# Optimization experiments

Measured on AMD Instinct MI355X. Metric: run time of the kernel, lower is better.

The kernel has to match this reference:

```python
import jax, jax.numpy as jnp
import numpy as np

N = 100000       # num nodes
E = 1000000      # num edges
D_IN = 128       # input feature dim
D_H = 64         # hidden = output dim
EPS = 1e-5       # GraphNorm eps
SLOPE = 0.2      # LeakyReLU negative slope


def _glorot(key, shape):
    lim = float(np.sqrt(6.0 / (shape[0] + shape[1])))
    return jax.random.uniform(key, shape, jnp.float32, -lim, lim)


def setup_inputs() -> dict:
    key = jax.random.key(0)
    ks = jax.random.split(key, 6)
    return {
        "x": jax.random.normal(ks[0], (N, D_IN), jnp.float32),
        "edge_index": jax.random.randint(ks[1], (2, E), 0, N),
        "W_in": _glorot(ks[2], (D_IN, D_H)),
        "b_in": jnp.zeros((D_H,), jnp.float32),
        "W1": _glorot(ks[3], (D_H, D_H)),
        "b1": jnp.zeros((D_H,), jnp.float32),
        "gn1_alpha": jnp.ones((D_H,), jnp.float32),
        "gn1_gamma": jnp.ones((D_H,), jnp.float32),
        "gn1_beta": jnp.zeros((D_H,), jnp.float32),
        "W2": _glorot(ks[4], (D_H, D_H)),
        "b2": jnp.zeros((D_H,), jnp.float32),
        "gn2_alpha": jnp.ones((D_H,), jnp.float32),
        "gn2_gamma": jnp.ones((D_H,), jnp.float32),
        "gn2_beta": jnp.zeros((D_H,), jnp.float32),
    }


def gcn_conv(x, W, b, src, dst):
    # GCNConv with added self-loops and symmetric normalization:
    # out = D^{-1/2} (A + I) D^{-1/2} (x W) + b
    xw = x @ W                                                 # [N, D]
    ones = jnp.ones((src.shape[0],), x.dtype)
    deg = jax.ops.segment_sum(ones, dst, num_segments=x.shape[0]) + 1.0  # +1 self-loop
    dinv = jax.lax.rsqrt(deg)                                  # [N]
    coef = dinv[src] * dinv[dst]                               # [E]
    agg = jax.ops.segment_sum(xw[src] * coef[:, None], dst, num_segments=x.shape[0])
    return agg + xw * (dinv * dinv)[:, None] + b


def graph_norm(x, alpha, gamma, beta):
    # PyG GraphNorm over a single graph: per-feature mean/var over all nodes
    mean = jnp.mean(x, axis=0)
    c = x - alpha * mean
    var = jnp.mean(c * c, axis=0)
    return gamma * c * jax.lax.rsqrt(var + EPS) + beta


def reference(x, edge_index, W_in, b_in, W1, b1, gn1_alpha, gn1_gamma, gn1_beta,
              W2, b2, gn2_alpha, gn2_gamma, gn2_beta):
    src, dst = edge_index[0], edge_index[1]
    h = x @ W_in + b_in                                        # input projection
    h = graph_norm(gcn_conv(h, W1, b1, src, dst), gn1_alpha, gn1_gamma, gn1_beta)
    h = jnp.where(h > 0, h, SLOPE * h)                         # LeakyReLU(0.2); dropout=eval (identity)
    h = graph_norm(gcn_conv(h, W2, b2, src, dst), gn2_alpha, gn2_gamma, gn2_beta)
    return h                                                    # [N, D_H]
```

## Files before the change

kernel.cpp:

```cpp
#include <hip/hip_runtime.h>
#include <stdint.h>
#include <string.h>

#define N_NODES 100000
#define N_EDGES 1000000
#define D_IN 128
#define D_H 64
#define EPS 1e-5f
#define SLOPE 0.2f

typedef unsigned short u16;
typedef unsigned int u32;
typedef __attribute__((ext_vector_type(8))) short bf16x8;
typedef __attribute__((ext_vector_type(4))) float f32x4;

__device__ __forceinline__ float bf2f(u16 u) {
    union { u32 i; float f; } v; v.i = ((u32)u) << 16; return v.f;
}
__device__ __forceinline__ u16 f2bf(float f) {
    union { float f; u32 i; } v; v.f = f;
    u32 r = (v.i + 0x7fffu + ((v.i >> 16) & 1u)) >> 16;
    return (u16)r;
}
__device__ __forceinline__ bool is_f32(const void* flagp) {
    return *(const u32*)flagp == 0x3F800000u;
}
__device__ __forceinline__ float loadf(const void* p, size_t i, bool m) {
    return m ? ((const float*)p)[i] : bf2f(((const u16*)p)[i]);
}

__global__ void kprep(const void* __restrict__ W_in, const void* __restrict__ b_in,
                      const void* __restrict__ W1, const void* __restrict__ W2,
                      const void* __restrict__ flagp,
                      u16* __restrict__ WcT, u16* __restrict__ W2T,
                      float* __restrict__ bc)
{
    bool m = is_f32(flagp);
    int t = threadIdx.x;
    if (blockIdx.x < 64) {
        int c = blockIdx.x;
        __shared__ float w1c[D_H];
        if (t < D_H) w1c[t] = loadf(W1, t * D_H + c, m);
        __syncthreads();
        float acc = 0.f;
        #pragma unroll 8
        for (int j = 0; j < D_H; j++) acc += loadf(W_in, t * D_H + j, m) * w1c[j];
        WcT[c * D_IN + t] = f2bf(acc);
        if (t == 0) {
            float b = 0.f;
            for (int j = 0; j < D_H; j++) b += loadf(b_in, j, m) * w1c[j];
            bc[c] = b;
        }
    } else {
        int idx = (blockIdx.x - 64) * 128 + t;
        int n = idx >> 6, k = idx & 63;
        W2T[n * D_H + k] = f2bf(loadf(W2, k * D_H + n, m));
    }
}

__global__ void kfill(const int* __restrict__ ei, int* __restrict__ cnt,
                      int* __restrict__ bucket)
{
    int e = blockIdx.x * blockDim.x + threadIdx.x;
    if (e >= N_EDGES) return;
    int s = ei[e];
    int d = ei[N_EDGES + e];
    int slot = atomicAdd(&cnt[d], 1);
    if (slot < 64) bucket[(size_t)d * 64 + slot] = s;
}

__global__ void kdinv(const int* __restrict__ cnt, float* __restrict__ dinv,
                      u16* __restrict__ xwb_pad)
{
    int i = blockIdx.x * blockDim.x + threadIdx.x;
    if (i < D_H) xwb_pad[(size_t)N_NODES * D_H + i] = 0;
    if (i >= N_NODES) return;
    dinv[i] = rsqrtf((float)cnt[i] + 1.0f);
}

__global__ __launch_bounds__(256) void kgemm1(const void* __restrict__ x,
        const u16* __restrict__ WcT, const float* __restrict__ bc,
        const float* __restrict__ dinv, const void* __restrict__ flagp,
        u16* __restrict__ xwb)
{
    bool m = is_f32(flagp);
    __shared__ __align__(16) u16 xs[64 * 136];
    __shared__ __align__(16) u16 WT[64 * 136];
    int tid = threadIdx.x;
    int row0 = blockIdx.x * 64;
    for (int i = tid; i < 64 * 32; i += 256) {
        int r = i >> 5, kq = (i & 31) * 4;
        *(ushort4*)(WT + r * 136 + kq) = *(const ushort4*)(WcT + r * D_IN + kq);
    }
    for (int i = tid; i < 64 * 32; i += 256) {
        int r = i >> 5, kq = (i & 31) * 4;
        int gr = row0 + r;
        ushort4 u = make_ushort4(0, 0, 0, 0);
        if (gr < N_NODES) {
            if (m) {
                float4 v = *(const float4*)((const float*)x + (size_t)gr * D_IN + kq);
                u = make_ushort4(f2bf(v.x), f2bf(v.y), f2bf(v.z), f2bf(v.w));
            } else {
                u = *(const ushort4*)((const u16*)x + (size_t)gr * D_IN + kq);
            }
        }
        *(ushort4*)(xs + r * 136 + kq) = u;
    }
    __syncthreads();
    int w = tid >> 6, L = tid & 63;
    int q = L >> 4, c = L & 15;
    f32x4 acc[4];
    #pragma unroll
    for (int ct = 0; ct < 4; ct++) {
        float b = bc[ct * 16 + c];
        acc[ct] = (f32x4){b, b, b, b};
    }
    const u16* ap = xs + (w * 16 + c) * 136 + q * 8;
    #pragma unroll
    for (int kk = 0; kk < 4; kk++) {
        bf16x8 af = *(const bf16x8*)(ap + kk * 32);
        #pragma unroll
        for (int ct = 0; ct < 4; ct++) {
            bf16x8 bfr = *(const bf16x8*)(WT + (ct * 16 + c) * 136 + kk * 32 + q * 8);
            acc[ct] = __builtin_amdgcn_mfma_f32_16x16x32_bf16(af, bfr, acc[ct], 0, 0, 0);
        }
    }
    #pragma unroll
    for (int r = 0; r < 4; r++) {
        int gr = row0 + w * 16 + q * 4 + r;
        if (gr < N_NODES) {
            float ds = dinv[gr];
            #pragma unroll
            for (int ct = 0; ct < 4; ct++)
                xwb[(size_t)gr * D_H + ct * 16 + c] = f2bf(acc[ct][r] * ds);
        }
    }
}

__global__ __launch_bounds__(256) void kagg(const u16* __restrict__ xwb,
        const float* __restrict__ dinv, const int* __restrict__ cnt,
        const int* __restrict__ bucket, const void* __restrict__ bvec,
        const void* __restrict__ flagp, u16* __restrict__ ybuf,
        float* __restrict__ accum)
{
    bool m = is_f32(flagp);
    __shared__ __align__(16) char smem[4][8192];
    __shared__ float red_s[4][64], red_q[4][64];
    int tid = threadIdx.x;
    int wv = tid >> 6, L = tid & 63;
    int half = L >> 5, mm = L & 31;
    int node0 = blockIdx.x * 32 + wv * 8;

    int cnt8 = cnt[node0 + (L & 7)];
    float di8 = dinv[node0 + (L & 7)];
    int deg[8]; float dd[8];
    #pragma unroll
    for (int t = 0; t < 8; t++) {
        deg[t] = min(__builtin_amdgcn_readlane(cnt8, t), 64);
        dd[t] = __uint_as_float(__builtin_amdgcn_readlane(__float_as_uint(di8), t));
    }
    float b0 = loadf(bvec, 2 * mm, m), b1 = loadf(bvec, 2 * mm + 1, m);

    float ls0 = 0, ls1 = 0, lq0 = 0, lq1 = 0;
    char* base = &smem[wv][0];

    #pragma unroll
    for (int b = 0; b < 2; b++) {
        int nb = node0 + b * 4;
        int tl = L >> 4, sl = L & 15;
        int i_l = nb + tl;
        int raw = bucket[(size_t)i_l * 64 + sl];
        int degL = min(__shfl(cnt8, b * 4 + tl), 64);
        int src = (sl < degL) ? raw : ((sl == degL) ? i_l : N_NODES);

        #pragma unroll
        for (int k = 0; k < 8; k++) {
            int srcK = __shfl(src, k * 8 + (L >> 3));
            const u16* gp = xwb + (size_t)srcK * D_H + (L & 7) * 8;
            __builtin_amdgcn_global_load_lds(gp, base + k * 1024, 16, 0, 0);
        }
        __builtin_amdgcn_s_waitcnt(0);
        __builtin_amdgcn_sched_barrier(0);
        asm volatile("" ::: "memory");

        float A0 = 0, A1 = 0, C0 = 0, C1 = 0;
        #pragma unroll
        for (int p = 0; p < 2; p++) {
            int np = p * 2 + half;
            const u32* rp = (const u32*)(base + np * 2048);
            float a0 = 0, a1 = 0;
            #pragma unroll
            for (int s = 0; s < 16; s++) {
                u32 v = rp[s * 32 + mm];
                a0 += __uint_as_float(v << 16);
                a1 += __uint_as_float(v & 0xffff0000u);
            }
            if (p == 0) { A0 = a0; A1 = a1; } else { C0 = a0; C1 = a1; }
        }
        #pragma unroll
        for (int t = 0; t < 4; t++) {
            int degt = deg[b * 4 + t];
            if (degt >= 16) {
                int i = nb + t;
                float r0 = 0, r1 = 0;
                for (int s = 16 + half; s <= degt; s += 2) {
                    int sv = (s < degt) ? bucket[(size_t)i * 64 + s] : i;
                    u32 v = *((const u32*)(xwb + (size_t)sv * D_H) + mm);
                    r0 += __uint_as_float(v << 16);
                    r1 += __uint_as_float(v & 0xffff0000u);
                }
                r0 += __shfl_xor(r0, 32);
                r1 += __shfl_xor(r1, 32);
                bool mine = (half == (t & 1));
                if (t < 2) { A0 += mine ? r0 : 0.f; A1 += mine ? r1 : 0.f; }
                else       { C0 += mine ? r0 : 0.f; C1 += mine ? r1 : 0.f; }
            }
        }
        #pragma unroll
        for (int p = 0; p < 2; p++) {
            float a0 = p ? C0 : A0, a1 = p ? C1 : A1;
            float ddv = half ? dd[b * 4 + p * 2 + 1] : dd[b * 4 + p * 2];
            float y0 = ddv * a0 + b0;
            float y1 = ddv * a1 + b1;
            int node = nb + p * 2 + half;
            ((u32*)(ybuf + (size_t)node * D_H))[mm] =
                (u32)f2bf(y0) | ((u32)f2bf(y1) << 16);
            ls0 += y0; ls1 += y1; lq0 += y0 * y0; lq1 += y1 * y1;
        }
        asm volatile("" ::: "memory");
    }

    ls0 += __shfl_xor(ls0, 32); ls1 += __shfl_xor(ls1, 32);
    lq0 += __shfl_xor(lq0, 32); lq1 += __shfl_xor(lq1, 32);
    if (half == 0) {
        *(float2*)&red_s[wv][2 * mm] = make_float2(ls0, ls1);
        *(float2*)&red_q[wv][2 * mm] = make_float2(lq0, lq1);
    }
    __syncthreads();
    if (tid < 64) {
        atomicAdd(&accum[tid],      red_s[0][tid] + red_s[1][tid] + red_s[2][tid] + red_s[3][tid]);
        atomicAdd(&accum[64 + tid], red_q[0][tid] + red_q[1][tid] + red_q[2][tid] + red_q[3][tid]);
    }
}

__global__ void kparams(const float* __restrict__ accum, const void* __restrict__ alpha,
        const void* __restrict__ gamma, const void* __restrict__ beta,
        const void* __restrict__ flagp, float* __restrict__ params)
{
    bool m = is_f32(flagp);
    int f = threadIdx.x;
    float mean = accum[f] * (1.0f / N_NODES);
    float al = loadf(alpha, f, m);
    float var = accum[64 + f] * (1.0f / N_NODES) - mean * mean * al * (2.0f - al);
    var = fmaxf(var, 0.f);
    float a = loadf(gamma, f, m) * rsqrtf(var + EPS);
    params[f] = a;
    params[64 + f] = loadf(beta, f, m) - a * al * mean;
}

__global__ __launch_bounds__(256) void kgemm2(const u16* __restrict__ y1b,
        const u16* __restrict__ W2T, const float* __restrict__ params,
        const float* __restrict__ dinv, u16* __restrict__ xwb)
{
    __shared__ __align__(16) u16 hs[64 * 72];
    __shared__ __align__(16) u16 WT[64 * 72];
    __shared__ float aL[64], cL[64];
    int tid = threadIdx.x;
    if (tid < 64) { aL[tid] = params[tid]; cL[tid] = params[64 + tid]; }
    for (int i = tid; i < 64 * 16; i += 256) {
        int r = i >> 4, kq = (i & 15) * 4;
        *(ushort4*)(WT + r * 72 + kq) = *(const ushort4*)(W2T + r * D_H + kq);
    }
    __syncthreads();
    int row0 = blockIdx.x * 64;
    for (int i = tid; i < 64 * 16; i += 256) {
        int r = i >> 4, kq = (i & 15) * 4;
        int gr = row0 + r;
        ushort4 u = make_ushort4(0, 0, 0, 0);
        if (gr < N_NODES) u = *(const ushort4*)(y1b + (size_t)gr * D_H + kq);
        float h0 = aL[kq + 0] * bf2f(u.x) + cL[kq + 0]; h0 = h0 > 0.f ? h0 : SLOPE * h0;
        float h1 = aL[kq + 1] * bf2f(u.y) + cL[kq + 1]; h1 = h1 > 0.f ? h1 : SLOPE * h1;
        float h2 = aL[kq + 2] * bf2f(u.z) + cL[kq + 2]; h2 = h2 > 0.f ? h2 : SLOPE * h2;
        float h3 = aL[kq + 3] * bf2f(u.w) + cL[kq + 3]; h3 = h3 > 0.f ? h3 : SLOPE * h3;
        *(ushort4*)(hs + r * 72 + kq) = make_ushort4(f2bf(h0), f2bf(h1), f2bf(h2), f2bf(h3));
    }
    __syncthreads();
    int w = tid >> 6, L = tid & 63;
    int q = L >> 4, c = L & 15;
    f32x4 acc[4] = {};
    const u16* ap = hs + (w * 16 + c) * 72 + q * 8;
    #pragma unroll
    for (int kk = 0; kk < 2; kk++) {
        bf16x8 af = *(const bf16x8*)(ap + kk * 32);
        #pragma unroll
        for (int ct = 0; ct < 4; ct++) {
            bf16x8 bfr = *(const bf16x8*)(WT + (ct * 16 + c) * 72 + kk * 32 + q * 8);
            acc[ct] = __builtin_amdgcn_mfma_f32_16x16x32_bf16(af, bfr, acc[ct], 0, 0, 0);
        }
    }
    #pragma unroll
    for (int r = 0; r < 4; r++) {
        int gr = row0 + w * 16 + q * 4 + r;
        if (gr < N_NODES) {
            float ds = dinv[gr];
            #pragma unroll
            for (int ct = 0; ct < 4; ct++)
                xwb[(size_t)gr * D_H + ct * 16 + c] = f2bf(acc[ct][r] * ds);
        }
    }
}

__global__ void kout(const u16* __restrict__ y2b, const float* __restrict__ params2,
                     const void* __restrict__ flagp, void* __restrict__ out)
{
    bool m = is_f32(flagp);
    int idx = blockIdx.x * blockDim.x + threadIdx.x;
    if (idx >= N_NODES * D_H) return;
    int f = idx & 63;
    float v = params2[f] * bf2f(y2b[idx]) + params2[64 + f];
    if (m) ((float*)out)[idx] = v;
    else   ((u16*)out)[idx] = f2bf(v);
}

extern "C" void kernel_launch(void* const* d_in, const int* in_sizes, int n_in,
                              void* d_out, int out_size, void* d_ws, size_t ws_size,
                              hipStream_t stream)
{
    const void* x    = d_in[0];
    const int*  ei   = (const int*)d_in[1];
    const void* W_in = d_in[2];
    const void* b_in = d_in[3];
    const void* W1   = d_in[4];
    const void* b1   = d_in[5];
    const void* gn1a = d_in[6];
    const void* gn1g = d_in[7];
    const void* gn1b = d_in[8];
    const void* W2   = d_in[9];
    const void* b2   = d_in[10];
    const void* gn2a = d_in[11];
    const void* gn2g = d_in[12];
    const void* gn2b = d_in[13];

    char* ws = (char*)d_ws;
    int*   cnt    = (int*)(ws + 0);
    float* accum  = (float*)(ws + 400000);
    float* params = (float*)(ws + 401024);
    float* bc     = (float*)(ws + 402048);
    u16*   WcT    = (u16*)(ws + 402432);
    u16*   W2T    = (u16*)(ws + 418816);
    float* dinv   = (float*)(ws + 435200);
    int*   bucket = (int*)(ws + 1235200);
    u16*   bufA   = (u16*)(ws + 26835200);
    u16*   bufB   = (u16*)(ws + 39635456);

    hipMemsetAsync(ws, 0, 400000 + 1024, stream);

    kprep<<<96, 128, 0, stream>>>(W_in, b_in, W1, W2, gn1a, WcT, W2T, bc);
    kfill<<<(N_EDGES + 255) / 256, 256, 0, stream>>>(ei, cnt, bucket);
    kdinv<<<(N_NODES + 255) / 256, 256, 0, stream>>>(cnt, dinv, bufA);
    kgemm1<<<(N_NODES + 63) / 64, 256, 0, stream>>>(x, WcT, bc, dinv, gn1a, bufA);
    kagg<<<N_NODES / 32, 256, 0, stream>>>(bufA, dinv, cnt, bucket, b1, gn1a, bufB, accum);
    kparams<<<1, 64, 0, stream>>>(accum, gn1a, gn1g, gn1b, gn1a, params);
    kgemm2<<<(N_NODES + 63) / 64, 256, 0, stream>>>(bufB, W2T, params, dinv, bufA);
    kagg<<<N_NODES / 32, 256, 0, stream>>>(bufA, dinv, cnt, bucket, b2, gn1a, bufB, accum + 128);
    kparams<<<1, 64, 0, stream>>>(accum + 128, gn2a, gn2g, gn2b, gn1a, params + 128);
    kout<<<(N_NODES * D_H + 255) / 256, 256, 0, stream>>>(bufB, params + 128, gn1a, d_out);
}
```

Baseline: 398.5 us.

## Remove dinv and params kernels, skip unused gather halves, vectorize output

Drops the kdinv and both kparams launches. Degree inverse-sqrt is now recomputed from cnt inside the GEMM and aggregation kernels, and the GraphNorm scale/shift is recomputed per block inside kgemm2 and kout. Aggregation hoists both bucket loads before the loop and skips the second 8-slot gather and its reduction when a node has at most 7 neighbours. kout now processes four outputs per thread with vector loads and stores. This removes launch overhead and wasted gathers, at the cost of some redundant per-block parameter math and more divergence in the gather loop.

```diff
diff --git a/kernel.cpp b/kernel.cpp
--- a/kernel.cpp
+++ b/kernel.cpp
@@ -1,6 +1,5 @@
 #include <hip/hip_runtime.h>
 #include <stdint.h>
-#include <string.h>
 
 #define N_NODES 100000
 #define N_EDGES 1000000
@@ -33,7 +32,7 @@
                       const void* __restrict__ W1, const void* __restrict__ W2,
                       const void* __restrict__ flagp,
                       u16* __restrict__ WcT, u16* __restrict__ W2T,
-                      float* __restrict__ bc)
+                      float* __restrict__ bc, u16* __restrict__ xwb_pad)
 {
     bool m = is_f32(flagp);
     int t = threadIdx.x;
@@ -51,6 +50,7 @@
             for (int j = 0; j < D_H; j++) b += loadf(b_in, j, m) * w1c[j];
             bc[c] = b;
         }
+        if (c == 0 && t < D_H) xwb_pad[(size_t)N_NODES * D_H + t] = 0;
     } else {
         int idx = (blockIdx.x - 64) * 128 + t;
         int n = idx >> 6, k = idx & 63;
@@ -69,18 +69,9 @@
     if (slot < 64) bucket[(size_t)d * 64 + slot] = s;
 }
 
-__global__ void kdinv(const int* __restrict__ cnt, float* __restrict__ dinv,
-                      u16* __restrict__ xwb_pad)
-{
-    int i = blockIdx.x * blockDim.x + threadIdx.x;
-    if (i < D_H) xwb_pad[(size_t)N_NODES * D_H + i] = 0;
-    if (i >= N_NODES) return;
-    dinv[i] = rsqrtf((float)cnt[i] + 1.0f);
-}
-
 __global__ __launch_bounds__(256) void kgemm1(const void* __restrict__ x,
         const u16* __restrict__ WcT, const float* __restrict__ bc,
-        const float* __restrict__ dinv, const void* __restrict__ flagp,
+        const int* __restrict__ cnt, const void* __restrict__ flagp,
         u16* __restrict__ xwb)
 {
     bool m = is_f32(flagp);
@@ -129,7 +120,7 @@
     for (int r = 0; r < 4; r++) {
         int gr = row0 + w * 16 + q * 4 + r;
         if (gr < N_NODES) {
-            float ds = dinv[gr];
+            float ds = rsqrtf((float)cnt[gr] + 1.0f);
             #pragma unroll
             for (int ct = 0; ct < 4; ct++)
                 xwb[(size_t)gr * D_H + ct * 16 + c] = f2bf(acc[ct][r] * ds);
@@ -138,10 +129,9 @@
 }
 
 __global__ __launch_bounds__(256) void kagg(const u16* __restrict__ xwb,
-        const float* __restrict__ dinv, const int* __restrict__ cnt,
-        const int* __restrict__ bucket, const void* __restrict__ bvec,
-        const void* __restrict__ flagp, u16* __restrict__ ybuf,
-        float* __restrict__ accum)
+        const int* __restrict__ cnt, const int* __restrict__ bucket,
+        const void* __restrict__ bvec, const void* __restrict__ flagp,
+        u16* __restrict__ ybuf, float* __restrict__ accum)
 {
     bool m = is_f32(flagp);
     __shared__ __align__(16) char smem[4][8192];
@@ -152,14 +142,18 @@
     int node0 = blockIdx.x * 32 + wv * 8;
 
     int cnt8 = cnt[node0 + (L & 7)];
-    float di8 = dinv[node0 + (L & 7)];
     int deg[8]; float dd[8];
     #pragma unroll
     for (int t = 0; t < 8; t++) {
-        deg[t] = min(__builtin_amdgcn_readlane(cnt8, t), 64);
-        dd[t] = __uint_as_float(__builtin_amdgcn_readlane(__float_as_uint(di8), t));
+        int cv = __builtin_amdgcn_readlane(cnt8, t);
+        deg[t] = min(cv, 64);
+        dd[t] = rsqrtf((float)cv + 1.0f);
     }
     float b0 = loadf(bvec, 2 * mm, m), b1 = loadf(bvec, 2 * mm + 1, m);
+
+    int tl = L >> 4, sl = L & 15;
+    int raw0 = bucket[(size_t)(node0 + tl) * 64 + sl];
+    int raw1 = bucket[(size_t)(node0 + 4 + tl) * 64 + sl];
 
     float ls0 = 0, ls1 = 0, lq0 = 0, lq1 = 0;
     char* base = &smem[wv][0];
@@ -167,17 +161,18 @@
     #pragma unroll
     for (int b = 0; b < 2; b++) {
         int nb = node0 + b * 4;
-        int tl = L >> 4, sl = L & 15;
+        int raw = b ? raw1 : raw0;
         int i_l = nb + tl;
-        int raw = bucket[(size_t)i_l * 64 + sl];
         int degL = min(__shfl(cnt8, b * 4 + tl), 64);
         int src = (sl < degL) ? raw : ((sl == degL) ? i_l : N_NODES);
 
         #pragma unroll
         for (int k = 0; k < 8; k++) {
-            int srcK = __shfl(src, k * 8 + (L >> 3));
-            const u16* gp = xwb + (size_t)srcK * D_H + (L & 7) * 8;
-            __builtin_amdgcn_global_load_lds(gp, base + k * 1024, 16, 0, 0);
+            if ((k & 1) == 0 || deg[b * 4 + (k >> 1)] + 1 > 8) {
+                int srcK = __shfl(src, k * 8 + (L >> 3));
+                const u16* gp = xwb + (size_t)srcK * D_H + (L & 7) * 8;
+                __builtin_amdgcn_global_load_lds(gp, base + k * 1024, 16, 0, 0);
+            }
         }
         __builtin_amdgcn_s_waitcnt(0);
         __builtin_amdgcn_sched_barrier(0);
@@ -188,12 +183,21 @@
         for (int p = 0; p < 2; p++) {
             int np = p * 2 + half;
             const u32* rp = (const u32*)(base + np * 2048);
+            int dnp = half ? deg[b * 4 + p * 2 + 1] : deg[b * 4 + p * 2];
             float a0 = 0, a1 = 0;
             #pragma unroll
-            for (int s = 0; s < 16; s++) {
+            for (int s = 0; s < 8; s++) {
                 u32 v = rp[s * 32 + mm];
                 a0 += __uint_as_float(v << 16);
                 a1 += __uint_as_float(v & 0xffff0000u);
+            }
+            if (dnp + 1 > 8) {
+                #pragma unroll
+                for (int s = 8; s < 16; s++) {
+                    u32 v = rp[s * 32 + mm];
+                    a0 += __uint_as_float(v << 16);
+                    a1 += __uint_as_float(v & 0xffff0000u);
+                }
             }
             if (p == 0) { A0 = a0; A1 = a1; } else { C0 = a0; C1 = a1; }
         }
@@ -243,30 +247,26 @@
     }
 }
 
-__global__ void kparams(const float* __restrict__ accum, const void* __restrict__ alpha,
-        const void* __restrict__ gamma, const void* __restrict__ beta,
-        const void* __restrict__ flagp, float* __restrict__ params)
-{
-    bool m = is_f32(flagp);
-    int f = threadIdx.x;
-    float mean = accum[f] * (1.0f / N_NODES);
-    float al = loadf(alpha, f, m);
-    float var = accum[64 + f] * (1.0f / N_NODES) - mean * mean * al * (2.0f - al);
-    var = fmaxf(var, 0.f);
-    float a = loadf(gamma, f, m) * rsqrtf(var + EPS);
-    params[f] = a;
-    params[64 + f] = loadf(beta, f, m) - a * al * mean;
-}
-
 __global__ __launch_bounds__(256) void kgemm2(const u16* __restrict__ y1b,
-        const u16* __restrict__ W2T, const float* __restrict__ params,
-        const float* __restrict__ dinv, u16* __restrict__ xwb)
-{
+        const u16* __restrict__ W2T, const float* __restrict__ accum,
+        const void* __restrict__ alpha, const void* __restrict__ gamma,
+        const void* __restrict__ beta, const void* __restrict__ flagp,
+        const int* __restrict__ cnt, u16* __restrict__ xwb)
+{
+    bool m = is_f32(flagp);
     __shared__ __align__(16) u16 hs[64 * 72];
     __shared__ __align__(16) u16 WT[64 * 72];
     __shared__ float aL[64], cL[64];
     int tid = threadIdx.x;
-    if (tid < 64) { aL[tid] = params[tid]; cL[tid] = params[64 + tid]; }
+    if (tid < 64) {
+        float mean = accum[tid] * (1.0f / N_NODES);
+        float al = loadf(alpha, tid, m);
+        float var = accum[64 + tid] * (1.0f / N_NODES) - mean * mean * al * (2.0f - al);
+        var = fmaxf(var, 0.f);
+        float a = loadf(gamma, tid, m) * rsqrtf(var + EPS);
+        aL[tid] = a;
+        cL[tid] = loadf(beta, tid, m) - a * al * mean;
+    }
     for (int i = tid; i < 64 * 16; i += 256) {
         int r = i >> 4, kq = (i & 15) * 4;
         *(ushort4*)(WT + r * 72 + kq) = *(const ushort4*)(W2T + r * D_H + kq);
@@ -302,7 +302,7 @@
     for (int r = 0; r < 4; r++) {
         int gr = row0 + w * 16 + q * 4 + r;
         if (gr < N_NODES) {
-            float ds = dinv[gr];
+            float ds = rsqrtf((float)cnt[gr] + 1.0f);
             #pragma unroll
             for (int ct = 0; ct < 4; ct++)
                 xwb[(size_t)gr * D_H + ct * 16 + c] = f2bf(acc[ct][r] * ds);
@@ -310,16 +310,39 @@
     }
 }
 
-__global__ void kout(const u16* __restrict__ y2b, const float* __restrict__ params2,
-                     const void* __restrict__ flagp, void* __restrict__ out)
-{
-    bool m = is_f32(flagp);
-    int idx = blockIdx.x * blockDim.x + threadIdx.x;
-    if (idx >= N_NODES * D_H) return;
-    int f = idx & 63;
-    float v = params2[f] * bf2f(y2b[idx]) + params2[64 + f];
-    if (m) ((float*)out)[idx] = v;
-    else   ((u16*)out)[idx] = f2bf(v);
+__global__ __launch_bounds__(256) void kout(const u16* __restrict__ y2b,
+        const float* __restrict__ accum2, const void* __restrict__ alpha,
+        const void* __restrict__ gamma, const void* __restrict__ beta,
+        const void* __restrict__ flagp, void* __restrict__ out)
+{
+    bool m = is_f32(flagp);
+    __shared__ float a2[64], c2[64];
+    int tid = threadIdx.x;
+    if (tid < 64) {
+        float mean = accum2[tid] * (1.0f / N_NODES);
+        float al = loadf(alpha, tid, m);
+        float var = accum2[64 + tid] * (1.0f / N_NODES) - mean * mean * al * (2.0f - al);
+        var = fmaxf(var, 0.f);
+        float a = loadf(gamma, tid, m) * rsqrtf(var + EPS);
+        a2[tid] = a;
+        c2[tid] = loadf(beta, tid, m) - a * al * mean;
+    }
+    __syncthreads();
+    int w0 = (blockIdx.x * 256 + tid) * 2;
+    u32 v0 = ((const u32*)y2b)[w0];
+    u32 v1 = ((const u32*)y2b)[w0 + 1];
+    int f = (w0 * 2) & 63;
+    float o0 = a2[f + 0] * __uint_as_float(v0 << 16)          + c2[f + 0];
+    float o1 = a2[f + 1] * __uint_as_float(v0 & 0xffff0000u)  + c2[f + 1];
+    float o2 = a2[f + 2] * __uint_as_float(v1 << 16)          + c2[f + 2];
+    float o3 = a2[f + 3] * __uint_as_float(v1 & 0xffff0000u)  + c2[f + 3];
+    if (m) {
+        *(float4*)((float*)out + (size_t)w0 * 2) = make_float4(o0, o1, o2, o3);
+    } else {
+        u32 p0 = (u32)f2bf(o0) | ((u32)f2bf(o1) << 16);
+        u32 p1 = (u32)f2bf(o2) | ((u32)f2bf(o3) << 16);
+        *(uint2*)((u32*)out + w0) = make_uint2(p0, p1);
+    }
 }
 
 extern "C" void kernel_launch(void* const* d_in, const int* in_sizes, int n_in,
@@ -344,25 +367,20 @@
     char* ws = (char*)d_ws;
     int*   cnt    = (int*)(ws + 0);
     float* accum  = (float*)(ws + 400000);
-    float* params = (float*)(ws + 401024);
     float* bc     = (float*)(ws + 402048);
     u16*   WcT    = (u16*)(ws + 402432);
     u16*   W2T    = (u16*)(ws + 418816);
-    float* dinv   = (float*)(ws + 435200);
     int*   bucket = (int*)(ws + 1235200);
     u16*   bufA   = (u16*)(ws + 26835200);
     u16*   bufB   = (u16*)(ws + 39635456);
 
     hipMemsetAsync(ws, 0, 400000 + 1024, stream);
 
-    kprep<<<96, 128, 0, stream>>>(W_in, b_in, W1, W2, gn1a, WcT, W2T, bc);
+    kprep<<<96, 128, 0, stream>>>(W_in, b_in, W1, W2, gn1a, WcT, W2T, bc, bufA);
     kfill<<<(N_EDGES + 255) / 256, 256, 0, stream>>>(ei, cnt, bucket);
-    kdinv<<<(N_NODES + 255) / 256, 256, 0, stream>>>(cnt, dinv, bufA);
-    kgemm1<<<(N_NODES + 63) / 64, 256, 0, stream>>>(x, WcT, bc, dinv, gn1a, bufA);
-    kagg<<<N_NODES / 32, 256, 0, stream>>>(bufA, dinv, cnt, bucket, b1, gn1a, bufB, accum);
-    kparams<<<1, 64, 0, stream>>>(accum, gn1a, gn1g, gn1b, gn1a, params);
-    kgemm2<<<(N_NODES + 63) / 64, 256, 0, stream>>>(bufB, W2T, params, dinv, bufA);
-    kagg<<<N_NODES / 32, 256, 0, stream>>>(bufA, dinv, cnt, bucket, b2, gn1a, bufB, accum + 128);
-    kparams<<<1, 64, 0, stream>>>(accum + 128, gn2a, gn2g, gn2b, gn1a, params + 128);
-    kout<<<(N_NODES * D_H + 255) / 256, 256, 0, stream>>>(bufB, params + 128, gn1a, d_out);
-}
+    kgemm1<<<(N_NODES + 63) / 64, 256, 0, stream>>>(x, WcT, bc, cnt, gn1a, bufA);
+    kagg<<<N_NODES / 32, 256, 0, stream>>>(bufA, cnt, bucket, b1, gn1a, bufB, accum);
+    kgemm2<<<(N_NODES + 63) / 64, 256, 0, stream>>>(bufB, W2T, accum, gn1a, gn1g, gn1b, gn1a, cnt, bufA);
+    kagg<<<N_NODES / 32, 256, 0, stream>>>(bufA, cnt, bucket, b2, gn1a, bufB, accum + 128);
+    kout<<<N_NODES * D_H / 1024, 256, 0, stream>>>(bufB, accum + 128, gn2a, gn2g, gn2b, gn1a, d_out);
+}
```

Result: no change. 398.3 us (-0.0%).
